# Kernel optimization log

Measured on AMD Instinct MI355X. Metric: run time of the kernel, lower is better.

Reference implementation:

```python
import jax, jax.numpy as jnp
import numpy as np

B, S, H, W = 16, 512, 768, 8


def _enumerate_spans(S, W):
    # same enumeration order as the torch triple loop: for i, for j in [i, min(i+W, S)-1]
    starts, widths = [], []
    for i in range(S):
        for w in range(1, min(W, S - i) + 1):
            starts.append(i)
            widths.append(w)
    return np.asarray(starts, np.int32), np.asarray(widths, np.int32)


def setup_inputs() -> dict:
    key = jax.random.key(0)
    k1, k2, k3 = jax.random.split(key, 3)
    embeddings = jax.random.normal(k1, (B, S, H), dtype=jnp.float32)
    w_lin = jax.random.normal(k2, (2 * H + 1, H), dtype=jnp.float32) * 0.02
    b_lin = jax.random.normal(k3, (H,), dtype=jnp.float32) * 0.02
    starts, widths = _enumerate_spans(S, W)
    return {
        "embeddings": embeddings,
        "w_lin": w_lin,
        "b_lin": b_lin,
        "span_starts": jnp.asarray(starts),
        "span_widths": jnp.asarray(widths),
    }


def reference(embeddings, w_lin, b_lin, span_starts, span_widths):
    Bb, Ss, Hh = embeddings.shape
    cls_emb = embeddings[:, 0, :]  # [B, H]

    # Sliding-window running max: pooled[k, b, i, :] = max(embeddings[b, i:i+k+1, :])
    neg = jnp.full((Bb, W - 1, Hh), -jnp.inf, embeddings.dtype)
    padded = jnp.concatenate([embeddings, neg], axis=1)  # [B, S+W-1, H]
    cm = embeddings
    pools = [cm]
    for k in range(1, W):
        cm = jnp.maximum(cm, padded[:, k:k + Ss, :])
        pools.append(cm)
    pooled = jnp.stack(pools, axis=0)  # [W, B, S, H]

    # Gather each span's max-pooled embedding: [N, B, H] -> [B, N, H]
    span_max = pooled[span_widths - 1, :, span_starts, :]
    span_max = jnp.transpose(span_max, (1, 0, 2))

    N = span_starts.shape[0]
    cls_b = jnp.broadcast_to(cls_emb[:, None, :], (Bb, N, Hh))
    width_f = jnp.broadcast_to(
        span_widths.astype(embeddings.dtype)[None, :, None], (Bb, N, 1))
    feats = jnp.concatenate([span_max, cls_b, width_f], axis=-1)  # [B, N, 2H+1]

    span_reps = jnp.einsum("bnf,fh->bnh", feats, w_lin) + b_lin
    token_inputs = cls_emb  # [B, H]
    return token_inputs, span_reps.reshape(Bb * N, Hh)
```

## Files before the change

kernel.cpp:

```cpp
#include <hip/hip_runtime.h>
#include <hip/hip_bf16.h>
#include <stdint.h>

#define AS1 __attribute__((address_space(1)))
#define AS3 __attribute__((address_space(3)))

typedef float  f32x4  __attribute__((ext_vector_type(4)));
typedef __bf16 bf16x8 __attribute__((ext_vector_type(8)));
typedef __bf16 bf16x4 __attribute__((ext_vector_type(4)));
typedef short  s16x8  __attribute__((ext_vector_type(8)));

static constexpr int Bc = 16, Sc = 512, Hc = 768, NSPAN = 4068;
static constexpr int BM = 128, BN = 256, BK = 64, KS = Hc / BK;

__global__ __launch_bounds__(256)
void prep_w1t(const float* __restrict__ w_lin, unsigned short* __restrict__ w1t) {
  __shared__ __align__(16) unsigned short T[64][80];
  int bidk = blockIdx.x % 12, bidn = blockIdx.x / 12;
  int k0 = bidk * 64, n0 = bidn * 64;
  int tid = threadIdx.x;
#pragma unroll
  for (int p = 0; p < 16; ++p) {
    int idx = p * 256 + tid;
    int kl = idx >> 6, nl = idx & 63;
    float v = w_lin[(size_t)(k0 + kl) * Hc + (n0 + nl)];
    __bf16 bv = (__bf16)v;
    T[nl][kl] = __builtin_bit_cast(unsigned short, bv);
  }
  __syncthreads();
#pragma unroll
  for (int qq = 0; qq < 2; ++qq) {
    int q = qq * 256 + tid;
    int nl = q >> 3, c = q & 7;
    int n = n0 + nl;
    int gp = (k0 >> 3) + (c ^ (n & 7));
    s16x8 v = *(const s16x8*)(&T[nl][c * 8]);
    *(s16x8*)(w1t + (size_t)n * Hc + gp * 8) = v;
  }
}

__global__ __launch_bounds__(256)
void cls_proj_kernel(const float* __restrict__ emb, const float* __restrict__ w_lin,
                     const float* __restrict__ b_lin, float* __restrict__ out,
                     float* __restrict__ cls_proj) {
  __shared__ float cls_s[Hc];
  int b = blockIdx.x / 3, hc = blockIdx.x % 3;
  int tid = threadIdx.x;
  const float* cls = emb + (size_t)b * Sc * Hc;
  for (int i = tid; i < Hc; i += 256) cls_s[i] = cls[i];
  __syncthreads();
  int h = hc * 256 + tid;
  const float* wp = w_lin + (size_t)Hc * Hc + h;
  float p0 = 0, p1 = 0, p2 = 0, p3 = 0, p4 = 0, p5 = 0, p6 = 0, p7 = 0;
  for (int f = 0; f < Hc; f += 8) {
    p0 += cls_s[f + 0] * wp[(size_t)(f + 0) * Hc];
    p1 += cls_s[f + 1] * wp[(size_t)(f + 1) * Hc];
    p2 += cls_s[f + 2] * wp[(size_t)(f + 2) * Hc];
    p3 += cls_s[f + 3] * wp[(size_t)(f + 3) * Hc];
    p4 += cls_s[f + 4] * wp[(size_t)(f + 4) * Hc];
    p5 += cls_s[f + 5] * wp[(size_t)(f + 5) * Hc];
    p6 += cls_s[f + 6] * wp[(size_t)(f + 6) * Hc];
    p7 += cls_s[f + 7] * wp[(size_t)(f + 7) * Hc];
  }
  float acc = b_lin[h] + (((p0 + p1) + (p2 + p3)) + ((p4 + p5) + (p6 + p7)));
  cls_proj[b * Hc + h] = acc;
  out[b * Hc + h] = cls_s[h];
}

__global__ __launch_bounds__(256, 2)
void span_gemm(const float* __restrict__ emb, const unsigned short* __restrict__ w1t,
               const float* __restrict__ cls_proj, const float* __restrict__ w_lin,
               float* __restrict__ out) {
  __shared__ __align__(16) unsigned short Ald[BM * BK];
  __shared__ __align__(16) unsigned short Bld[BN * BK];

  int bid = blockIdx.x;
  int tile_n = bid % 3, tile_m = bid / 3;
  int b = tile_m >> 5;
  int s0 = (tile_m & 31) << 4;
  int n0 = tile_n * BN;
  int tid = threadIdx.x;
  int wid = tid >> 6, lane = tid & 63;
  int lq = lane >> 4, lr = lane & 15;

  const char* embC = (const char*)(emb + (size_t)b * Sc * Hc);

  int bi = tid >> 4, bkq = tid & 15;
  uint32_t rowoff[8];
#pragma unroll
  for (int t = 0; t < 8; ++t) {
    int r = s0 + bi + t;
    if (r > 511) r = 511;
    rowoff[t] = (uint32_t)r * (Hc * 4) + bkq * 16;
  }
  int awbase = (bi << 10) + ((bkq & 1) << 3);

  f32x4 acc[8][4];
  f32x4 zer = {0.f, 0.f, 0.f, 0.f};
#pragma unroll
  for (int i = 0; i < 8; ++i)
#pragma unroll
    for (int j = 0; j < 4; ++j) acc[i][j] = zer;

  for (int ks = 0; ks < KS; ++ks) {
    int k0 = ks * BK;

    f32x4 rv[8];
#pragma unroll
    for (int t = 0; t < 8; ++t)
      rv[t] = *(const f32x4*)(embC + rowoff[t] + k0 * 4);

    __syncthreads();

#pragma unroll
    for (int j = 0; j < 8; ++j) {
      int u = (wid << 3) + j;
      int n = n0 + (u << 3) + (lane >> 3);
      const unsigned short* gp = w1t + (size_t)n * Hc + k0 + ((lane & 7) << 3);
      __builtin_amdgcn_global_load_lds((const AS1 uint32_t*)gp,
                                       (AS3 uint32_t*)(Bld + (u << 9)), 16, 0, 0);
    }

    {
      f32x4 cm = rv[0];
#pragma unroll
      for (int t = 0; t < 8; ++t) {
        if (t) {
          cm[0] = fmaxf(cm[0], rv[t][0]);
          cm[1] = fmaxf(cm[1], rv[t][1]);
          cm[2] = fmaxf(cm[2], rv[t][2]);
          cm[3] = fmaxf(cm[3], rv[t][3]);
        }
        bf16x4 p;
        p[0] = (__bf16)cm[0]; p[1] = (__bf16)cm[1];
        p[2] = (__bf16)cm[2]; p[3] = (__bf16)cm[3];
        int off = awbase + (t << 7) + ((((bkq >> 1) ^ t)) << 4);
        *(uint2*)((char*)Ald + off) = __builtin_bit_cast(uint2, p);
      }
    }

    __syncthreads();

#pragma unroll
    for (int kk = 0; kk < 2; ++kk) {
      bf16x8 af[8], bfr[4];
      int cf = (kk << 2) + lq;
#pragma unroll
      for (int mi = 0; mi < 8; ++mi) {
        int m = (mi << 4) + lr;
        af[mi] = *(const bf16x8*)((const char*)Ald + (m << 7) + ((cf ^ (m & 7)) << 4));
      }
#pragma unroll
      for (int ni = 0; ni < 4; ++ni) {
        int n = (wid << 6) + (ni << 4) + lr;
        bfr[ni] = *(const bf16x8*)((const char*)Bld + (n << 7) + ((cf ^ (n & 7)) << 4));
      }
#pragma unroll
      for (int mi = 0; mi < 8; ++mi)
#pragma unroll
        for (int ni = 0; ni < 4; ++ni)
          acc[mi][ni] = __builtin_amdgcn_mfma_f32_16x16x32_bf16(af[mi], bfr[ni], acc[mi][ni], 0, 0, 0);
    }
  }

  const float* w2p = w_lin + (size_t)(2 * Hc) * Hc;
  float* outp = out + Bc * Hc;
  int swb = (tile_m & 31) << 7;
#pragma unroll
  for (int ni = 0; ni < 4; ++ni) {
    int h = n0 + (wid << 6) + (ni << 4) + lr;
    float cp = cls_proj[b * Hc + h];
    float w2 = w2p[h];
#pragma unroll
    for (int mi = 0; mi < 8; ++mi) {
#pragma unroll
      for (int j = 0; j < 4; ++j) {
        int m = (mi << 4) + (lq << 2) + j;
        int sw = swb + m;
        int s = sw >> 3, w = (sw & 7) + 1;
        if (s + w <= 512) {
          int nsp = (s <= 504) ? (sw)
                               : (NSPAN - (((512 - s) * (513 - s)) >> 1) + w - 1);
          size_t oidx = ((size_t)b * NSPAN + nsp) * Hc + h;
          outp[oidx] = acc[mi][ni][j] + cp + (float)w * w2;
        }
      }
    }
  }
}

extern "C" void kernel_launch(void* const* d_in, const int* in_sizes, int n_in,
                              void* d_out, int out_size, void* d_ws, size_t ws_size,
                              hipStream_t stream) {
  const float* emb = (const float*)d_in[0];
  const float* w_lin = (const float*)d_in[1];
  const float* b_lin = (const float*)d_in[2];
  unsigned short* w1t = (unsigned short*)d_ws;
  float* cls_proj = (float*)((char*)d_ws + (size_t)Hc * Hc * 2);
  float* out = (float*)d_out;

  hipLaunchKernelGGL(prep_w1t, dim3(144), dim3(256), 0, stream, w_lin, w1t);
  hipLaunchKernelGGL(cls_proj_kernel, dim3(48), dim3(256), 0, stream, emb, w_lin, b_lin, out, cls_proj);
  hipLaunchKernelGGL(span_gemm, dim3(512 * 3), dim3(256), 0, stream, emb, w1t, cls_proj, w_lin, out);
}
```

Measured before the change: 127.5 us.

## Double-buffer A tile in LDS and load B fragments directly into registers

Moves the B operand (transposed bf16 weight) out of LDS: each wave now loads its MFMA B fragments straight from global memory into registers, and the weight prep no longer applies an XOR swizzle. The A tile (sliding-window max of embeddings) is double-buffered in LDS and software-pipelined, with embedding loads for step k+2 and B loads for step k+1 issued while step k computes. This leaves one barrier per k-step instead of two. The cost is higher register pressure from the prefetched rv and bfr arrays, and uncoalesced per-lane 16-byte global loads for B, which each wave repeats without sharing through LDS.

```diff
diff --git a/kernel.cpp b/kernel.cpp
--- a/kernel.cpp
+++ b/kernel.cpp
@@ -1,9 +1,6 @@
 #include <hip/hip_runtime.h>
 #include <hip/hip_bf16.h>
 #include <stdint.h>
-
-#define AS1 __attribute__((address_space(1)))
-#define AS3 __attribute__((address_space(3)))
 
 typedef float  f32x4  __attribute__((ext_vector_type(4)));
 typedef __bf16 bf16x8 __attribute__((ext_vector_type(8)));
@@ -33,9 +30,8 @@
     int q = qq * 256 + tid;
     int nl = q >> 3, c = q & 7;
     int n = n0 + nl;
-    int gp = (k0 >> 3) + (c ^ (n & 7));
     s16x8 v = *(const s16x8*)(&T[nl][c * 8]);
-    *(s16x8*)(w1t + (size_t)n * Hc + gp * 8) = v;
+    *(s16x8*)(w1t + (size_t)n * Hc + k0 + c * 8) = v;
   }
 }
 
@@ -71,8 +67,7 @@
 void span_gemm(const float* __restrict__ emb, const unsigned short* __restrict__ w1t,
                const float* __restrict__ cls_proj, const float* __restrict__ w_lin,
                float* __restrict__ out) {
-  __shared__ __align__(16) unsigned short Ald[BM * BK];
-  __shared__ __align__(16) unsigned short Bld[BN * BK];
+  __shared__ __align__(16) unsigned short Ald[2][BM * BK];
 
   int bid = blockIdx.x;
   int tile_n = bid % 3, tile_m = bid / 3;
@@ -95,6 +90,8 @@
   }
   int awbase = (bi << 10) + ((bkq & 1) << 3);
 
+  const unsigned short* bbase = w1t + (size_t)(n0 + (wid << 6) + lr) * Hc + (lq << 3);
+
   f32x4 acc[8][4];
   f32x4 zer = {0.f, 0.f, 0.f, 0.f};
 #pragma unroll
@@ -102,64 +99,74 @@
 #pragma unroll
     for (int j = 0; j < 4; ++j) acc[i][j] = zer;
 
+  f32x4 rv[8];
+  bf16x8 bfr[4][2];
+
+#define BUILD_A(dstbuf)                                                        \
+  {                                                                            \
+    f32x4 cm = rv[0];                                                          \
+    _Pragma("unroll") for (int t = 0; t < 8; ++t) {                            \
+      if (t) {                                                                 \
+        cm[0] = fmaxf(cm[0], rv[t][0]);                                        \
+        cm[1] = fmaxf(cm[1], rv[t][1]);                                        \
+        cm[2] = fmaxf(cm[2], rv[t][2]);                                        \
+        cm[3] = fmaxf(cm[3], rv[t][3]);                                        \
+      }                                                                        \
+      bf16x4 p;                                                                \
+      p[0] = (__bf16)cm[0]; p[1] = (__bf16)cm[1];                              \
+      p[2] = (__bf16)cm[2]; p[3] = (__bf16)cm[3];                              \
+      int off = awbase + (t << 7) + ((((bkq >> 1) ^ t)) << 4);                 \
+      *(uint2*)((char*)(dstbuf) + off) = __builtin_bit_cast(uint2, p);         \
+    }                                                                          \
+  }
+
+#pragma unroll
+  for (int t = 0; t < 8; ++t) rv[t] = *(const f32x4*)(embC + rowoff[t]);
+  BUILD_A(Ald[0]);
+#pragma unroll
+  for (int t = 0; t < 8; ++t) rv[t] = *(const f32x4*)(embC + rowoff[t] + 256);
+#pragma unroll
+  for (int ni = 0; ni < 4; ++ni)
+#pragma unroll
+    for (int kk = 0; kk < 2; ++kk)
+      bfr[ni][kk] = *(const bf16x8*)(bbase + ni * 16 * Hc + kk * 32);
+  asm volatile("s_waitcnt lgkmcnt(0)" ::: "memory");
+  __builtin_amdgcn_sched_barrier(0);
+  __builtin_amdgcn_s_barrier();
+
   for (int ks = 0; ks < KS; ++ks) {
-    int k0 = ks * BK;
-
-    f32x4 rv[8];
-#pragma unroll
-    for (int t = 0; t < 8; ++t)
-      rv[t] = *(const f32x4*)(embC + rowoff[t] + k0 * 4);
-
-    __syncthreads();
-
-#pragma unroll
-    for (int j = 0; j < 8; ++j) {
-      int u = (wid << 3) + j;
-      int n = n0 + (u << 3) + (lane >> 3);
-      const unsigned short* gp = w1t + (size_t)n * Hc + k0 + ((lane & 7) << 3);
-      __builtin_amdgcn_global_load_lds((const AS1 uint32_t*)gp,
-                                       (AS3 uint32_t*)(Bld + (u << 9)), 16, 0, 0);
-    }
-
-    {
-      f32x4 cm = rv[0];
-#pragma unroll
-      for (int t = 0; t < 8; ++t) {
-        if (t) {
-          cm[0] = fmaxf(cm[0], rv[t][0]);
-          cm[1] = fmaxf(cm[1], rv[t][1]);
-          cm[2] = fmaxf(cm[2], rv[t][2]);
-          cm[3] = fmaxf(cm[3], rv[t][3]);
-        }
-        bf16x4 p;
-        p[0] = (__bf16)cm[0]; p[1] = (__bf16)cm[1];
-        p[2] = (__bf16)cm[2]; p[3] = (__bf16)cm[3];
-        int off = awbase + (t << 7) + ((((bkq >> 1) ^ t)) << 4);
-        *(uint2*)((char*)Ald + off) = __builtin_bit_cast(uint2, p);
-      }
-    }
-
-    __syncthreads();
-
+    const char* abuf = (const char*)Ald[ks & 1];
 #pragma unroll
     for (int kk = 0; kk < 2; ++kk) {
-      bf16x8 af[8], bfr[4];
+      bf16x8 af[8];
       int cf = (kk << 2) + lq;
 #pragma unroll
       for (int mi = 0; mi < 8; ++mi) {
         int m = (mi << 4) + lr;
-        af[mi] = *(const bf16x8*)((const char*)Ald + (m << 7) + ((cf ^ (m & 7)) << 4));
+        af[mi] = *(const bf16x8*)(abuf + (m << 7) + ((cf ^ (m & 7)) << 4));
       }
 #pragma unroll
-      for (int ni = 0; ni < 4; ++ni) {
-        int n = (wid << 6) + (ni << 4) + lr;
-        bfr[ni] = *(const bf16x8*)((const char*)Bld + (n << 7) + ((cf ^ (n & 7)) << 4));
+      for (int mi = 0; mi < 8; ++mi)
+#pragma unroll
+        for (int ni = 0; ni < 4; ++ni)
+          acc[mi][ni] = __builtin_amdgcn_mfma_f32_16x16x32_bf16(af[mi], bfr[ni][kk], acc[mi][ni], 0, 0, 0);
+    }
+
+    if (ks < KS - 1) {
+      BUILD_A(Ald[(ks + 1) & 1]);
+      if (ks < KS - 2) {
+#pragma unroll
+        for (int t = 0; t < 8; ++t)
+          rv[t] = *(const f32x4*)(embC + rowoff[t] + (ks + 2) * 256);
       }
 #pragma unroll
-      for (int mi = 0; mi < 8; ++mi)
-#pragma unroll
-        for (int ni = 0; ni < 4; ++ni)
-          acc[mi][ni] = __builtin_amdgcn_mfma_f32_16x16x32_bf16(af[mi], bfr[ni], acc[mi][ni], 0, 0, 0);
+      for (int ni = 0; ni < 4; ++ni)
+#pragma unroll
+        for (int kk = 0; kk < 2; ++kk)
+          bfr[ni][kk] = *(const bf16x8*)(bbase + ni * 16 * Hc + (ks + 1) * 64 + kk * 32);
+      asm volatile("s_waitcnt lgkmcnt(0)" ::: "memory");
+      __builtin_amdgcn_sched_barrier(0);
+      __builtin_amdgcn_s_barrier();
     }
   }
 
```

New measurement: 150.2 us. +17.8%, slower.
